# Optimization experiments

Measured on AMD Instinct MI355X. Metric: run time of the kernel, lower is better.

The kernel has to match this reference:

```python
import jax, jax.numpy as jnp
import numpy as np

N_NODES = 50000
N_EDGES = 300000
DIM = 256
ALPHA = 0.1  # residual mixing with initial features, as passed in forward


def gcn_layer(x0, x, edge_idx, W):
    """One GraphConvolution call: mean neighbor aggregation over the edge
    list, GCNII-style residual mix with initial features x0, then linear."""
    src, dst = edge_idx[0], edge_idx[1]
    msgs = x[src]  # [E, D] gather
    agg = jax.ops.segment_sum(msgs, dst, num_segments=x.shape[0])
    deg = jax.ops.segment_sum(jnp.ones((src.shape[0],), x.dtype), dst,
                              num_segments=x.shape[0])
    agg = agg / jnp.maximum(deg, 1.0)[:, None]
    h = ALPHA * x0 + (1.0 - ALPHA) * agg
    return h @ W


def setup_inputs() -> dict:
    key = jax.random.key(0)
    k1, k2, k3 = jax.random.split(key, 3)
    x = jax.random.normal(k1, (N_NODES, DIM), dtype=jnp.float32)
    edge_idx = jax.random.randint(k2, (2, N_EDGES), 0, N_NODES, dtype=jnp.int64)
    W = jax.random.normal(k3, (DIM, DIM), dtype=jnp.float32) / np.sqrt(DIM)
    return {"drug_cell_pair_feature": x, "edge_idx": edge_idx, "W": W}


def reference(drug_cell_pair_feature, edge_idx, W):
    x0 = drug_cell_pair_feature
    out = jax.nn.relu(gcn_layer(x0, x0, edge_idx, W))
    for _ in range(4):  # 4 more identical calls, always mixing with x0
        out = jax.nn.relu(gcn_layer(x0, out, edge_idx, W))
    return out
```

## Files before the change

kernel.cpp:

```cpp
#include <hip/hip_runtime.h>

#define DIM 256
#define SCAN_B 256

typedef __attribute__((ext_vector_type(8))) short short8;
typedef __attribute__((ext_vector_type(8))) unsigned short u16x8;
typedef __attribute__((ext_vector_type(4))) float f32x4;

__device__ __forceinline__ unsigned short f32_to_bf16(float x) {
    unsigned int u = __float_as_uint(x);
    unsigned int r = u + 0x7FFFu + ((u >> 16) & 1u);
    return (unsigned short)(r >> 16);
}
__device__ __forceinline__ float bf16_to_f32(unsigned short h) {
    return __uint_as_float(((unsigned int)h) << 16);
}

__device__ __forceinline__ void load_lds16(const void* g, void* l) {
    __builtin_amdgcn_global_load_lds(
        (const __attribute__((address_space(1))) unsigned int*)g,
        (__attribute__((address_space(3))) unsigned int*)l, 16, 0, 0);
}

__global__ void deg_kernel(const int* __restrict__ dst, int E, int* __restrict__ deg) {
    int e = blockIdx.x * blockDim.x + threadIdx.x;
    if (e < E) atomicAdd(&deg[dst[e]], 1);
}

__global__ void scan1_kernel(const int* __restrict__ deg, int N,
                             int* __restrict__ excl, int* __restrict__ bsums) {
    __shared__ int s[SCAN_B];
    int tid = threadIdx.x;
    int i = blockIdx.x * SCAN_B + tid;
    int v = (i < N) ? deg[i] : 0;
    s[tid] = v;
    __syncthreads();
    #pragma unroll
    for (int off = 1; off < SCAN_B; off <<= 1) {
        int t = (tid >= off) ? s[tid - off] : 0;
        __syncthreads();
        s[tid] += t;
        __syncthreads();
    }
    if (i <= N) excl[i] = s[tid] - v;
    if (tid == SCAN_B - 1) bsums[blockIdx.x] = s[tid];
}

__global__ void scan2_kernel(int* __restrict__ bsums, int nb) {
    __shared__ int s[SCAN_B];
    int tid = threadIdx.x;
    int v = (tid < nb) ? bsums[tid] : 0;
    s[tid] = v;
    __syncthreads();
    #pragma unroll
    for (int off = 1; off < SCAN_B; off <<= 1) {
        int t = (tid >= off) ? s[tid - off] : 0;
        __syncthreads();
        s[tid] += t;
        __syncthreads();
    }
    if (tid < nb) bsums[tid] = s[tid] - v;
}

__global__ void scan3_kernel(const int* __restrict__ excl, const int* __restrict__ bsums,
                             const int* __restrict__ deg, int N,
                             int* __restrict__ row_start, float* __restrict__ inv_deg) {
    int i = blockIdx.x * SCAN_B + threadIdx.x;
    if (i <= N) row_start[i] = excl[i] + bsums[blockIdx.x];
    if (i < N) inv_deg[i] = 1.0f / (float)max(deg[i], 1);
}

__global__ void fill_kernel(const int* __restrict__ src, const int* __restrict__ dst, int E,
                            const int* __restrict__ row_start, int* __restrict__ cursor,
                            int* __restrict__ csr_src) {
    int e = blockIdx.x * blockDim.x + threadIdx.x;
    if (e < E) {
        int d = dst[e];
        int pos = row_start[d] + atomicAdd(&cursor[d], 1);
        csr_src[pos] = src[e];
    }
}

__global__ void prep_kernel(const float* __restrict__ W, unsigned short* __restrict__ Wt,
                            const float* __restrict__ x0, unsigned short* __restrict__ x0b,
                            int n4) {
    int b = blockIdx.x;
    if (b < DIM) {
        int k = b, n = threadIdx.x;
        Wt[n * DIM + k] = f32_to_bf16(W[k * DIM + n]);
    } else {
        int i = (b - DIM) * 256 + threadIdx.x;
        if (i < n4) {
            float4 v = ((const float4*)x0)[i];
            ushort4 o;
            o.x = f32_to_bf16(v.x); o.y = f32_to_bf16(v.y);
            o.z = f32_to_bf16(v.z); o.w = f32_to_bf16(v.w);
            ((ushort4*)x0b)[i] = o;
        }
    }
}

__global__ __launch_bounds__(256) void aggregate_kernel(
    const unsigned short* __restrict__ xh, const unsigned short* __restrict__ x0b,
    const int* __restrict__ row_start, const int* __restrict__ csr_src,
    const float* __restrict__ inv_deg,
    unsigned short* __restrict__ h, int N)
{
    int node = blockIdx.x * 4 + (threadIdx.x >> 6);
    if (node >= N) return;
    const int lane = threadIdx.x & 63;
    const int half = lane >> 5;
    const int c    = (lane & 31) * 8;

    int beg = row_start[node];
    int end = row_start[node + 1];

    float a[8];
    #pragma unroll
    for (int j = 0; j < 8; j++) a[j] = 0.f;

    int e = beg;
    for (; e + 4 <= end; e += 4) {
        int s0 = csr_src[e + half];
        int s1 = csr_src[e + 2 + half];
        u16x8 v0 = *(const u16x8*)(xh + (size_t)s0 * DIM + c);
        u16x8 v1 = *(const u16x8*)(xh + (size_t)s1 * DIM + c);
        #pragma unroll
        for (int j = 0; j < 8; j++) a[j] += bf16_to_f32(v0[j]) + bf16_to_f32(v1[j]);
    }
    if (e + 2 <= end) {
        int s0 = csr_src[e + half];
        u16x8 v0 = *(const u16x8*)(xh + (size_t)s0 * DIM + c);
        #pragma unroll
        for (int j = 0; j < 8; j++) a[j] += bf16_to_f32(v0[j]);
        e += 2;
    }
    if (e < end && half == 0) {
        int s0 = csr_src[e];
        u16x8 v0 = *(const u16x8*)(xh + (size_t)s0 * DIM + c);
        #pragma unroll
        for (int j = 0; j < 8; j++) a[j] += bf16_to_f32(v0[j]);
    }

    #pragma unroll
    for (int j = 0; j < 8; j++) a[j] += __shfl_xor(a[j], 32);

    if (half == 0) {
        float scale = 0.9f * inv_deg[node];
        u16x8 xv = *(const u16x8*)(x0b + (size_t)node * DIM + c);
        u16x8 o;
        #pragma unroll
        for (int j = 0; j < 8; j++)
            o[j] = f32_to_bf16(0.1f * bf16_to_f32(xv[j]) + scale * a[j]);
        *(u16x8*)(h + (size_t)node * DIM + c) = o;
    }
}

template <bool LAST>
__global__ __launch_bounds__(256) void gemm_kernel(
    const unsigned short* __restrict__ h, const unsigned short* __restrict__ Wt,
    float* __restrict__ out_f32, unsigned short* __restrict__ out_bf16, int N)
{
    __shared__ unsigned short As[128 * 32];
    __shared__ unsigned short Bs[128 * 32];

    const int t    = threadIdx.x;
    const int w    = t >> 6;
    const int lane = t & 63;
    const int lm   = lane & 15;
    const int q    = lane >> 4;
    const int wm   = w >> 1, wn = w & 1;
    const int m0   = blockIdx.x * 128;
    const int n0   = blockIdx.y * 128;

    const int sr = t >> 2;
    const int sg = (t & 3) * 8;

    f32x4 acc[4][4];
    #pragma unroll
    for (int mi = 0; mi < 4; mi++)
        #pragma unroll
        for (int ni = 0; ni < 4; ni++)
            acc[mi][ni] = (f32x4){0.f, 0.f, 0.f, 0.f};

    for (int kb = 0; kb < DIM; kb += 32) {
        __syncthreads();
        #pragma unroll
        for (int half = 0; half < 2; half++) {
            int r = half * 64 + sr;
            int ldso = (half * 256 + t) * 8;
            load_lds16(h  + (size_t)(m0 + r) * DIM + kb + sg, &As[ldso]);
            load_lds16(Wt + (size_t)(n0 + r) * DIM + kb + sg, &Bs[ldso]);
        }
        __syncthreads();

        short8 a[4];
        #pragma unroll
        for (int mi = 0; mi < 4; mi++) {
            int row = wm * 64 + mi * 16 + lm;
            a[mi] = *(const short8*)&As[row * 32 + q * 8];
        }
        #pragma unroll
        for (int ni = 0; ni < 4; ni++) {
            int row = wn * 64 + ni * 16 + lm;
            short8 b = *(const short8*)&Bs[row * 32 + q * 8];
            #pragma unroll
            for (int mi = 0; mi < 4; mi++)
                acc[mi][ni] = __builtin_amdgcn_mfma_f32_16x16x32_bf16(a[mi], b, acc[mi][ni], 0, 0, 0);
        }
    }

    #pragma unroll
    for (int mi = 0; mi < 4; mi++) {
        const int rowb = m0 + wm * 64 + mi * 16 + q * 4;
        #pragma unroll
        for (int ni = 0; ni < 4; ni++) {
            const int col = n0 + wn * 64 + ni * 16 + lm;
            #pragma unroll
            for (int r = 0; r < 4; r++) {
                int row = rowb + r;
                if (row < N) {
                    float v = fmaxf(acc[mi][ni][r], 0.0f);
                    if (LAST) out_f32[(size_t)row * DIM + col] = v;
                    else      out_bf16[(size_t)row * DIM + col] = f32_to_bf16(v);
                }
            }
        }
    }
}

extern "C" void kernel_launch(void* const* d_in, const int* in_sizes, int n_in,
                              void* d_out, int out_size, void* d_ws, size_t ws_size,
                              hipStream_t stream) {
    const float* x0  = (const float*)d_in[0];
    const int*   ei  = (const int*)d_in[1];
    const float* W   = (const float*)d_in[2];
    float*       out = (float*)d_out;

    const int N = in_sizes[0] / DIM;
    const int E = in_sizes[1] / 2;
    const int N_pad = (N + 127) & ~127;
    const int* src = ei;
    const int* dst = ei + E;

    const int nb = (N + 1 + SCAN_B - 1) / SCAN_B;

    char* ws = (char*)d_ws;
    size_t off = 0;
    auto alloc = [&](size_t bytes) { char* p = ws + off; off += (bytes + 15) & ~size_t(15); return p; };
    unsigned short* h       = (unsigned short*)alloc((size_t)N_pad * DIM * 2);
    unsigned short* act     = (unsigned short*)alloc((size_t)N_pad * DIM * 2);
    unsigned short* x0b     = (unsigned short*)alloc((size_t)N_pad * DIM * 2);
    unsigned short* Wt      = (unsigned short*)alloc((size_t)DIM * DIM * 2);
    float* inv_deg  = (float*)alloc((size_t)N * 4);
    int*   deg      = (int*)  alloc((size_t)N * 4 * 2);
    int*   cursor   = deg + N;
    int*   row_start= (int*)  alloc((size_t)(N + 1) * 4);
    int*   excl     = (int*)  alloc((size_t)(N + 1) * 4);
    int*   bsums    = (int*)  alloc((size_t)nb * 4);
    int*   csr_src  = (int*)  alloc((size_t)E * 4);

    hipMemsetAsync(deg, 0, (size_t)N * 4 * 2, stream);
    deg_kernel<<<(E + 255) / 256, 256, 0, stream>>>(dst, E, deg);
    scan1_kernel<<<nb, SCAN_B, 0, stream>>>(deg, N, excl, bsums);
    scan2_kernel<<<1, SCAN_B, 0, stream>>>(bsums, nb);
    scan3_kernel<<<nb, SCAN_B, 0, stream>>>(excl, bsums, deg, N, row_start, inv_deg);
    fill_kernel<<<(E + 255) / 256, 256, 0, stream>>>(src, dst, E, row_start, cursor, csr_src);
    const int n4 = N * DIM / 4;
    prep_kernel<<<DIM + (n4 + 255) / 256, 256, 0, stream>>>(W, Wt, x0, x0b, n4);

    dim3 ggrid(N_pad / 128, 2);
    for (int layer = 0; layer < 5; layer++) {
        const unsigned short* gsrc = (layer == 0) ? x0b : act;
        aggregate_kernel<<<(N + 3) / 4, 256, 0, stream>>>(gsrc, x0b, row_start, csr_src,
                                                          inv_deg, h, N);
        if (layer == 4)
            gemm_kernel<true><<<ggrid, 256, 0, stream>>>(h, Wt, out, nullptr, N);
        else
            gemm_kernel<false><<<ggrid, 256, 0, stream>>>(h, Wt, nullptr, act, N);
    }
}
```

Baseline: 380.8 us.

## Fuse degree/prep kernels, half-wave per node aggregation, LDS-free direct-load GEMM

Merges the degree-count kernel with the weight-transpose and x0 bf16 conversion into one launch, removing a kernel launch. The aggregation now assigns each half-wavefront its own node, processing 8 nodes per block. Each half loops over all of its node's edges with 4-way unrolled gathers, which removes the cross-half shuffle reduction. The GEMM drops LDS staging and barriers and loads MFMA operands straight from global memory, relying on cache reuse. The risk is redundant global loads across waves and worse balance across nodes of uneven degree.

```diff
diff --git a/kernel.cpp b/kernel.cpp
--- a/kernel.cpp
+++ b/kernel.cpp
@@ -16,15 +16,27 @@
     return __uint_as_float(((unsigned int)h) << 16);
 }
 
-__device__ __forceinline__ void load_lds16(const void* g, void* l) {
-    __builtin_amdgcn_global_load_lds(
-        (const __attribute__((address_space(1))) unsigned int*)g,
-        (__attribute__((address_space(3))) unsigned int*)l, 16, 0, 0);
-}
-
-__global__ void deg_kernel(const int* __restrict__ dst, int E, int* __restrict__ deg) {
-    int e = blockIdx.x * blockDim.x + threadIdx.x;
-    if (e < E) atomicAdd(&deg[dst[e]], 1);
+__global__ void degprep_kernel(const int* __restrict__ dst, int E, int* __restrict__ deg,
+                               const float* __restrict__ W, unsigned short* __restrict__ Wt,
+                               const float* __restrict__ x0, unsigned short* __restrict__ x0b,
+                               int n4, int nbdeg) {
+    int b = blockIdx.x;
+    if (b < nbdeg) {
+        int e = b * 256 + threadIdx.x;
+        if (e < E) atomicAdd(&deg[dst[e]], 1);
+    } else if (b < nbdeg + DIM) {
+        int k = b - nbdeg, n = threadIdx.x;
+        Wt[n * DIM + k] = f32_to_bf16(W[k * DIM + n]);
+    } else {
+        int i = (b - nbdeg - DIM) * 256 + threadIdx.x;
+        if (i < n4) {
+            float4 v = ((const float4*)x0)[i];
+            ushort4 o;
+            o.x = f32_to_bf16(v.x); o.y = f32_to_bf16(v.y);
+            o.z = f32_to_bf16(v.z); o.w = f32_to_bf16(v.w);
+            ((ushort4*)x0b)[i] = o;
+        }
+    }
 }
 
 __global__ void scan1_kernel(const int* __restrict__ deg, int N,
@@ -81,39 +93,28 @@
     }
 }
 
-__global__ void prep_kernel(const float* __restrict__ W, unsigned short* __restrict__ Wt,
-                            const float* __restrict__ x0, unsigned short* __restrict__ x0b,
-                            int n4) {
-    int b = blockIdx.x;
-    if (b < DIM) {
-        int k = b, n = threadIdx.x;
-        Wt[n * DIM + k] = f32_to_bf16(W[k * DIM + n]);
-    } else {
-        int i = (b - DIM) * 256 + threadIdx.x;
-        if (i < n4) {
-            float4 v = ((const float4*)x0)[i];
-            ushort4 o;
-            o.x = f32_to_bf16(v.x); o.y = f32_to_bf16(v.y);
-            o.z = f32_to_bf16(v.z); o.w = f32_to_bf16(v.w);
-            ((ushort4*)x0b)[i] = o;
-        }
-    }
-}
-
 __global__ __launch_bounds__(256) void aggregate_kernel(
     const unsigned short* __restrict__ xh, const unsigned short* __restrict__ x0b,
     const int* __restrict__ row_start, const int* __restrict__ csr_src,
     const float* __restrict__ inv_deg,
     unsigned short* __restrict__ h, int N)
 {
-    int node = blockIdx.x * 4 + (threadIdx.x >> 6);
-    if (node >= N) return;
     const int lane = threadIdx.x & 63;
     const int half = lane >> 5;
+    const int node = blockIdx.x * 8 + ((threadIdx.x >> 6) << 1) + half;
     const int c    = (lane & 31) * 8;
 
-    int beg = row_start[node];
-    int end = row_start[node + 1];
+    int beg = 0, end = 0;
+    float dscale = 0.f;
+    u16x8 xv;
+    #pragma unroll
+    for (int j = 0; j < 8; j++) xv[j] = 0;
+    if (node < N) {
+        beg = row_start[node];
+        end = row_start[node + 1];
+        dscale = 0.9f * inv_deg[node];
+        xv = *(const u16x8*)(x0b + (size_t)node * DIM + c);
+    }
 
     float a[8];
     #pragma unroll
@@ -121,37 +122,37 @@
 
     int e = beg;
     for (; e + 4 <= end; e += 4) {
-        int s0 = csr_src[e + half];
-        int s1 = csr_src[e + 2 + half];
+        int s0 = csr_src[e], s1 = csr_src[e + 1], s2 = csr_src[e + 2], s3 = csr_src[e + 3];
         u16x8 v0 = *(const u16x8*)(xh + (size_t)s0 * DIM + c);
         u16x8 v1 = *(const u16x8*)(xh + (size_t)s1 * DIM + c);
-        #pragma unroll
-        for (int j = 0; j < 8; j++) a[j] += bf16_to_f32(v0[j]) + bf16_to_f32(v1[j]);
+        u16x8 v2 = *(const u16x8*)(xh + (size_t)s2 * DIM + c);
+        u16x8 v3 = *(const u16x8*)(xh + (size_t)s3 * DIM + c);
+        #pragma unroll
+        for (int j = 0; j < 8; j++)
+            a[j] += (bf16_to_f32(v0[j]) + bf16_to_f32(v1[j]))
+                  + (bf16_to_f32(v2[j]) + bf16_to_f32(v3[j]));
     }
     if (e + 2 <= end) {
-        int s0 = csr_src[e + half];
+        int s0 = csr_src[e], s1 = csr_src[e + 1];
         u16x8 v0 = *(const u16x8*)(xh + (size_t)s0 * DIM + c);
-        #pragma unroll
-        for (int j = 0; j < 8; j++) a[j] += bf16_to_f32(v0[j]);
+        u16x8 v1 = *(const u16x8*)(xh + (size_t)s1 * DIM + c);
+        #pragma unroll
+        for (int j = 0; j < 8; j++)
+            a[j] += bf16_to_f32(v0[j]) + bf16_to_f32(v1[j]);
         e += 2;
     }
-    if (e < end && half == 0) {
+    if (e < end) {
         int s0 = csr_src[e];
         u16x8 v0 = *(const u16x8*)(xh + (size_t)s0 * DIM + c);
         #pragma unroll
         for (int j = 0; j < 8; j++) a[j] += bf16_to_f32(v0[j]);
     }
 
-    #pragma unroll
-    for (int j = 0; j < 8; j++) a[j] += __shfl_xor(a[j], 32);
-
-    if (half == 0) {
-        float scale = 0.9f * inv_deg[node];
-        u16x8 xv = *(const u16x8*)(x0b + (size_t)node * DIM + c);
+    if (node < N) {
         u16x8 o;
         #pragma unroll
         for (int j = 0; j < 8; j++)
-            o[j] = f32_to_bf16(0.1f * bf16_to_f32(xv[j]) + scale * a[j]);
+            o[j] = f32_to_bf16(0.1f * bf16_to_f32(xv[j]) + dscale * a[j]);
         *(u16x8*)(h + (size_t)node * DIM + c) = o;
     }
 }
@@ -161,9 +162,6 @@
     const unsigned short* __restrict__ h, const unsigned short* __restrict__ Wt,
     float* __restrict__ out_f32, unsigned short* __restrict__ out_bf16, int N)
 {
-    __shared__ unsigned short As[128 * 32];
-    __shared__ unsigned short Bs[128 * 32];
-
     const int t    = threadIdx.x;
     const int w    = t >> 6;
     const int lane = t & 63;
@@ -173,8 +171,8 @@
     const int m0   = blockIdx.x * 128;
     const int n0   = blockIdx.y * 128;
 
-    const int sr = t >> 2;
-    const int sg = (t & 3) * 8;
+    const unsigned short* Ab = h  + (size_t)(m0 + wm * 64 + lm) * DIM + q * 8;
+    const unsigned short* Bb = Wt + (size_t)(n0 + wn * 64 + lm) * DIM + q * 8;
 
     f32x4 acc[4][4];
     #pragma unroll
@@ -183,31 +181,20 @@
         for (int ni = 0; ni < 4; ni++)
             acc[mi][ni] = (f32x4){0.f, 0.f, 0.f, 0.f};
 
-    for (int kb = 0; kb < DIM; kb += 32) {
-        __syncthreads();
-        #pragma unroll
-        for (int half = 0; half < 2; half++) {
-            int r = half * 64 + sr;
-            int ldso = (half * 256 + t) * 8;
-            load_lds16(h  + (size_t)(m0 + r) * DIM + kb + sg, &As[ldso]);
-            load_lds16(Wt + (size_t)(n0 + r) * DIM + kb + sg, &Bs[ldso]);
-        }
-        __syncthreads();
-
-        short8 a[4];
-        #pragma unroll
-        for (int mi = 0; mi < 4; mi++) {
-            int row = wm * 64 + mi * 16 + lm;
-            a[mi] = *(const short8*)&As[row * 32 + q * 8];
-        }
-        #pragma unroll
-        for (int ni = 0; ni < 4; ni++) {
-            int row = wn * 64 + ni * 16 + lm;
-            short8 b = *(const short8*)&Bs[row * 32 + q * 8];
+    #pragma unroll
+    for (int ks = 0; ks < 8; ks++) {
+        short8 a[4], b[4];
+        #pragma unroll
+        for (int mi = 0; mi < 4; mi++)
+            a[mi] = *(const short8*)(Ab + (size_t)mi * 16 * DIM + ks * 32);
+        #pragma unroll
+        for (int ni = 0; ni < 4; ni++)
+            b[ni] = *(const short8*)(Bb + (size_t)ni * 16 * DIM + ks * 32);
+        #pragma unroll
+        for (int ni = 0; ni < 4; ni++)
             #pragma unroll
             for (int mi = 0; mi < 4; mi++)
-                acc[mi][ni] = __builtin_amdgcn_mfma_f32_16x16x32_bf16(a[mi], b, acc[mi][ni], 0, 0, 0);
-        }
+                acc[mi][ni] = __builtin_amdgcn_mfma_f32_16x16x32_bf16(a[mi], b[ni], acc[mi][ni], 0, 0, 0);
     }
 
     #pragma unroll
@@ -260,19 +247,20 @@
     int*   bsums    = (int*)  alloc((size_t)nb * 4);
     int*   csr_src  = (int*)  alloc((size_t)E * 4);
 
+    const int nbdeg = (E + 255) / 256;
+    const int n4 = N * DIM / 4;
     hipMemsetAsync(deg, 0, (size_t)N * 4 * 2, stream);
-    deg_kernel<<<(E + 255) / 256, 256, 0, stream>>>(dst, E, deg);
+    degprep_kernel<<<nbdeg + DIM + (n4 + 255) / 256, 256, 0, stream>>>(
+        dst, E, deg, W, Wt, x0, x0b, n4, nbdeg);
     scan1_kernel<<<nb, SCAN_B, 0, stream>>>(deg, N, excl, bsums);
     scan2_kernel<<<1, SCAN_B, 0, stream>>>(bsums, nb);
     scan3_kernel<<<nb, SCAN_B, 0, stream>>>(excl, bsums, deg, N, row_start, inv_deg);
     fill_kernel<<<(E + 255) / 256, 256, 0, stream>>>(src, dst, E, row_start, cursor, csr_src);
-    const int n4 = N * DIM / 4;
-    prep_kernel<<<DIM + (n4 + 255) / 256, 256, 0, stream>>>(W, Wt, x0, x0b, n4);
 
     dim3 ggrid(N_pad / 128, 2);
     for (int layer = 0; layer < 5; layer++) {
         const unsigned short* gsrc = (layer == 0) ? x0b : act;
-        aggregate_kernel<<<(N + 3) / 4, 256, 0, stream>>>(gsrc, x0b, row_start, csr_src,
+        aggregate_kernel<<<(N + 7) / 8, 256, 0, stream>>>(gsrc, x0b, row_start, csr_src,
                                                           inv_deg, h, N);
         if (layer == 4)
             gemm_kernel<true><<<ggrid, 256, 0, stream>>>(h, Wt, out, nullptr, N);
```

Measured after the change: 452.5 us. 18.9% more time.
